# Kernel optimization log

Measured on AMD Instinct MI355X. Metric: run time of the kernel, lower is better.

The kernel has to match this reference:

```python
import jax, jax.numpy as jnp
from jax import lax
import numpy as np

B, IMG, PS = 64, 384, 16
DM, DS, DI = 96, 16, 96
DT_RANK = 6
NREP = 4
NCLS = 5
HP = IMG // PS            # 24 patches per side
N = HP * HP               # 576 tokens


def _ln(x, g, b):
    m = x.mean(-1, keepdims=True)
    v = ((x - m) ** 2).mean(-1, keepdims=True)
    return (x - m) * lax.rsqrt(v + 1e-5) * g + b


def setup_inputs() -> dict:
    key = jax.random.key(0)
    ks = jax.random.split(key, 16)
    nrm = lambda k, s: jax.random.normal(k, s, jnp.float32) * 0.02
    return {
        "x": jax.random.uniform(ks[0], (B, 3, IMG, IMG), jnp.float32),
        "W_pe": nrm(ks[1], (DM, 3, PS, PS)), "b_pe": jnp.zeros((DM,), jnp.float32),
        "W_vis": nrm(ks[2], (DM, 1)), "b_vis": jnp.zeros((1,), jnp.float32),
        "dn_g": jnp.ones((DM,), jnp.float32), "dn_b": jnp.zeros((DM,), jnp.float32),
        "W_gate": nrm(ks[3], (DM, DM)), "b_gate": jnp.zeros((DM,), jnp.float32),
        "ln_g": jnp.ones((DM,), jnp.float32), "ln_b": jnp.zeros((DM,), jnp.float32),
        "W_in": nrm(ks[4], (DM, 2 * DI)),
        "conv_w": nrm(ks[5], (DI, 1, 3)),
        "W_xproj": nrm(ks[6], (DI, DT_RANK + 2 * DS)),
        "W_dt": nrm(ks[7], (DT_RANK, DI)), "b_dt": jnp.full((DI,), -2.0, jnp.float32),
        "A_log": jnp.log(jnp.tile(jnp.arange(1, DS + 1, dtype=jnp.float32), (DI, 1))),
        "D": jnp.ones((DI,), jnp.float32),
        "W_out": nrm(ks[8], (DI, DM)),
        "hd_dw": nrm(ks[9], (DM, 1, 3, 3)),
        "bn_g": jnp.ones((DM,), jnp.float32), "bn_b": jnp.zeros((DM,), jnp.float32),
        "bn_m": jnp.zeros((DM,), jnp.float32), "bn_v": jnp.ones((DM,), jnp.float32),
        "W_heat": nrm(ks[10], (NCLS, DM)), "b_heat": jnp.full((NCLS,), -2.19, jnp.float32),
        "W_off": nrm(ks[11], (2, DM)), "b_off": jnp.zeros((2,), jnp.float32),
        "W_size": nrm(ks[12], (2, DM)), "b_size": jnp.zeros((2,), jnp.float32),
    }


def _forward(x, W_pe, b_pe, W_vis, b_vis, dn_g, dn_b, W_gate, b_gate,
             ln_g, ln_b, W_in, conv_w, W_xproj, W_dt, b_dt, A_log, D, W_out,
             hd_dw, bn_g, bn_b, bn_m, bn_v, W_heat, b_heat, W_off, b_off, W_size, b_size):
    # --- retinex preprocessing (single-scale, log domain) ---
    kblur = jnp.ones((3, 1, 5, 5), jnp.float32) / 25.0
    L = lax.conv_general_dilated(x, kblur, (1, 1), 'SAME',
                                 feature_group_count=3,
                                 dimension_numbers=('NCHW', 'OIHW', 'NCHW'))
    x = jnp.log1p(jnp.clip(x, 0.0)) - jnp.log1p(jnp.clip(L, 0.0))
    # --- patch embedding: strided conv -> tokens (B,N,DM) ---
    t = lax.conv_general_dilated(x, W_pe, (PS, PS), 'VALID',
                                 dimension_numbers=('NCHW', 'OIHW', 'NCHW'))
    t = t + b_pe[None, :, None, None]
    tokens = t.reshape(B, DM, N).transpose(0, 2, 1)
    # --- visibility estimator: per-token gate (B,N,1) ---
    vis = jax.nn.sigmoid(tokens @ W_vis + b_vis)
    # --- dual norm: LN + sigmoid gate ---
    tokens = _ln(tokens, dn_g, dn_b)
    norm_gate = jax.nn.sigmoid(tokens @ W_gate + b_gate)  # (B,N,DM)
    # --- weight-shared NC-SSM blocks ---
    A = -jnp.exp(A_log)  # (DI,DS)
    for _ in range(NREP):
        resid = tokens
        h = _ln(tokens, ln_g, ln_b)
        xz = h @ W_in                      # (B,N,2*DI)
        xin, z = xz[..., :DI], xz[..., DI:]
        # causal depthwise conv1d over sequence, kernel 3
        xc = xin.transpose(0, 2, 1)        # (B,DI,N)
        xc = lax.conv_general_dilated(xc, conv_w, (1,), [(2, 0)],
                                      feature_group_count=DI,
                                      dimension_numbers=('NCH', 'OIH', 'NCH'))
        xs = jax.nn.silu(xc.transpose(0, 2, 1))  # (B,N,DI)
        # selective-scan parameters
        proj = xs @ W_xproj                # (B,N,DT_RANK+2*DS)
        dt_raw = proj[..., :DT_RANK]
        Bc = proj[..., DT_RANK:DT_RANK + DS]
        Cc = proj[..., DT_RANK + DS:]
        dt = jax.nn.softplus(dt_raw @ W_dt + b_dt)  # (B,N,DI)
        # time-major scan
        def step(hst, inp):
            dt_t, B_t, C_t, x_t = inp      # (B,DI),(B,DS),(B,DS),(B,DI)
            dA = jnp.exp(dt_t[:, :, None] * A)                 # (B,DI,DS)
            hst = dA * hst + (dt_t * x_t)[:, :, None] * B_t[:, None, :]
            y = jnp.einsum('bds,bs->bd', hst, C_t)
            return hst, y
        h0 = jnp.zeros((B, DI, DS), jnp.float32)
        _, ys = lax.scan(step, h0, (dt.transpose(1, 0, 2), Bc.transpose(1, 0, 2),
                                    Cc.transpose(1, 0, 2), xs.transpose(1, 0, 2)))
        y = ys.transpose(1, 0, 2) + D * xs           # (B,N,DI)
        y = y * jax.nn.silu(z) * vis                  # gated by z and visibility
        tokens = resid + (y @ W_out) * norm_gate
    # --- CenterNet-style head ---
    f = tokens.transpose(0, 2, 1).reshape(B, DM, HP, HP)
    g = lax.conv_general_dilated(f, hd_dw, (1, 1), 'SAME',
                                 feature_group_count=DM,
                                 dimension_numbers=('NCHW', 'OIHW', 'NCHW'))
    g = (g - bn_m[None, :, None, None]) * lax.rsqrt(bn_v + 1e-5)[None, :, None, None]
    g = jax.nn.silu(g * bn_g[None, :, None, None] + bn_b[None, :, None, None])
    heat = jnp.einsum('bchw,oc->bohw', g, W_heat) + b_heat[None, :, None, None]
    off = jnp.einsum('bchw,oc->bohw', f, W_off) + b_off[None, :, None, None]
    size = jnp.einsum('bchw,oc->bohw', f, W_size) + b_size[None, :, None, None]
    return heat, off, size


def reference(x, W_pe, b_pe, W_vis, b_vis, dn_g, dn_b, W_gate, b_gate,
              ln_g, ln_b, W_in, conv_w, W_xproj, W_dt, b_dt, A_log, D, W_out,
              hd_dw, bn_g, bn_b, bn_m, bn_v, W_heat, b_heat, W_off, b_off, W_size, b_size):
    return _forward(x, W_pe, b_pe, W_vis, b_vis, dn_g, dn_b, W_gate, b_gate,
                    ln_g, ln_b, W_in, conv_w, W_xproj, W_dt, b_dt, A_log, D, W_out,
                    hd_dw, bn_g, bn_b, bn_m, bn_v, W_heat, b_heat, W_off, b_off,
                    W_size, b_size)
```

## Files before the change

kernel.cpp:

```cpp
#include <hip/hip_runtime.h>

#define DEVINL __device__ __forceinline__

typedef __attribute__((ext_vector_type(8))) short bf8v;
typedef __attribute__((ext_vector_type(4))) float f4v;

DEVINL float b2f(unsigned short u){ union{unsigned int i; float f;} x; x.i = ((unsigned int)u)<<16; return x.f; }
DEVINL unsigned short f2b(float f){ union{float f; unsigned int i;} x; x.f = f; unsigned int r = x.i + 0x7FFFu + ((x.i>>16)&1u); return (unsigned short)(r>>16); }
DEVINL float sigf(float v){ return 1.f/(1.f + __expf(-v)); }
DEVINL void unpack8(const uint4 u, float* d){
  d[0]=b2f((unsigned short)(u.x)); d[1]=b2f((unsigned short)(u.x>>16));
  d[2]=b2f((unsigned short)(u.y)); d[3]=b2f((unsigned short)(u.y>>16));
  d[4]=b2f((unsigned short)(u.z)); d[5]=b2f((unsigned short)(u.z>>16));
  d[6]=b2f((unsigned short)(u.w)); d[7]=b2f((unsigned short)(u.w>>16));
}
DEVINL uint4 pack8(const float* s){
  uint4 u;
  u.x = (unsigned int)f2b(s[0]) | ((unsigned int)f2b(s[1])<<16);
  u.y = (unsigned int)f2b(s[2]) | ((unsigned int)f2b(s[3])<<16);
  u.z = (unsigned int)f2b(s[4]) | ((unsigned int)f2b(s[5])<<16);
  u.w = (unsigned int)f2b(s[6]) | ((unsigned int)f2b(s[7])<<16);
  return u;
}
union FragU { uint4 u; bf8v v; };


#define WS_XLOG   ((size_t)0)
#define WS_TOK    ((size_t)56623104)
#define WS_VIS    ((size_t)70778880)
#define WS_WGT    ((size_t)70926336)
#define WS_WIT    ((size_t)70944768)
#define WS_WXT    ((size_t)70981632)
#define WS_WOT    ((size_t)71006208)
#define WS_AMAT   ((size_t)71024640)
#define WS_WPE    ((size_t)71030784)
#define WS_CW     ((size_t)71178240)
#define WS_BC     ((size_t)0)
#define WS_GATE   ((size_t)14155776)
#define WS_XSB    ((size_t)21233664)
#define WS_Y2     ((size_t)28311552)
#define WS_XIN    ((size_t)35389440)
#define WS_ZSV    ((size_t)42467328)
#define WS_DT     ((size_t)49545216)

#define PREP_STRIDE (128*256)
__global__ __launch_bounds__(256) void k_prep(
    const float* __restrict__ Wgate, const float* __restrict__ Win,
    const float* __restrict__ Wxproj, const float* __restrict__ Wdt,
    const float* __restrict__ Wout, const float* __restrict__ Alog,
    const float* __restrict__ Wpe, const float* __restrict__ convw,
    unsigned short* __restrict__ WgT, unsigned short* __restrict__ WiT,
    unsigned short* __restrict__ WxT, unsigned short* __restrict__ WoT,
    float* __restrict__ Amat, unsigned short* __restrict__ WpeB,
    float* __restrict__ cwsplit)
{
  int gtid = blockIdx.x*256 + threadIdx.x;
  for (int i = gtid; i < 9216; i += PREP_STRIDE){
    int n = i/96, k = i - n*96;
    WgT[n*96+k] = f2b(Wgate[k*96+n]);
    WoT[n*96+k] = f2b(Wout[k*96+n]);
  }
  for (int i = gtid; i < 18432; i += PREP_STRIDE){
    int n = i/96, k = i - n*96;
    WiT[n*96+k] = f2b(Win[k*192+n]);
  }
  for (int i = gtid; i < 12288; i += PREP_STRIDE){
    int n = i/96, k = i - n*96;
    if (n < 96){
      float s = 0.f;
      for (int r = 0; r < 6; ++r) s += Wxproj[k*38+r] * Wdt[r*96+n];
      WxT[n*96+k] = f2b(s);
    } else {
      WxT[n*96+k] = f2b(Wxproj[k*38 + 6 + (n-96)]);
    }
  }
  for (int i = gtid; i < 1536; i += PREP_STRIDE) Amat[i] = -__expf(Alog[i]);
  for (int i = gtid; i < 73728; i += PREP_STRIDE) WpeB[i] = f2b(Wpe[i]);
  for (int i = gtid; i < 96; i += PREP_STRIDE){
    cwsplit[i]       = convw[i*3+0];
    cwsplit[96+i]    = convw[i*3+1];
    cwsplit[192+i]   = convw[i*3+2];
  }
}

__global__ __launch_bounds__(256) void k_blur(const float* __restrict__ x,
                                              unsigned short* __restrict__ xlog)
{
  __shared__ unsigned short xt[12*384];
  __shared__ float vt[8*392];
  int bid = blockIdx.x;
  int tile = bid % 48; int bc = bid / 48; int c = bc % 3; int b = bc / 3;
  const float* xin = x + (size_t)(b*3 + c) * 147456;
  unsigned short* xout = xlog + (size_t)(b*3 + c) * 147456;
  int y0 = tile * 8;
  int tid = threadIdx.x;

  #pragma unroll
  for (int k = 0; k < 5; ++k){
    int idx = tid + k*256;
    if (idx < 1152){
      int r = idx / 96; int c4 = idx - r*96;
      int gy = y0 - 2 + r;
      float4 v = make_float4(0.f,0.f,0.f,0.f);
      if (gy >= 0 && gy < 384) v = *(const float4*)(xin + gy*384 + c4*4);
      ushort4 o; o.x=f2b(v.x); o.y=f2b(v.y); o.z=f2b(v.z); o.w=f2b(v.w);
      *(ushort4*)(xt + r*384 + c4*4) = o;
    }
  }
  if (tid < 64){
    int r = tid >> 3; int j = tid & 7;
    vt[r*392 + ((j < 4) ? j : (384 + j))] = 0.f;
  }
  __syncthreads();

  #pragma unroll
  for (int k = 0; k < 2; ++k){
    int unit = tid + k*256;
    if (unit < 384){
      int r = unit / 48; int c8 = unit - r*48;
      const unsigned short* base = xt + r*384 + c8*8;
      float acc[8]; float t[8];
      uint4 u0 = *(const uint4*)(base);
      unpack8(u0, acc);
      #pragma unroll
      for (int i = 1; i < 5; ++i){
        uint4 u = *(const uint4*)(base + i*384);
        unpack8(u, t);
        #pragma unroll
        for (int j = 0; j < 8; ++j) acc[j] += t[j];
      }
      float* vrow = vt + r*392 + 4 + c8*8;
      *(float4*)(vrow)   = make_float4(acc[0],acc[1],acc[2],acc[3]);
      *(float4*)(vrow+4) = make_float4(acc[4],acc[5],acc[6],acc[7]);
    }
  }
  __syncthreads();

  #pragma unroll
  for (int k = 0; k < 3; ++k){
    int unit = tid + k*256;
    int r = unit / 96; int c4 = unit - r*96;
    int base = r*392 + 4 + c4*4;
    float f[12];
    *(float4*)(f)   = *(const float4*)(vt + base - 4);
    *(float4*)(f+4) = *(const float4*)(vt + base);
    *(float4*)(f+8) = *(const float4*)(vt + base + 4);
    ushort4 xr = *(const ushort4*)(xt + (r+2)*384 + c4*4);
    const unsigned short* xrp = &xr.x;
    ushort4 o;
    unsigned short* op = &o.x;
    #pragma unroll
    for (int j = 0; j < 4; ++j){
      float s = f[2+j] + f[3+j] + f[4+j] + f[5+j] + f[6+j];
      float L = fmaxf(s * 0.04f, 0.f);
      float xv = fmaxf(b2f(xrp[j]), 0.f);
      op[j] = f2b(__logf(1.f + xv) - __logf(1.f + L));
    }
    *(ushort4*)(xout + (y0+r)*384 + c4*4) = o;
  }
}

__global__ __launch_bounds__(256) void k_patchln(
    const unsigned short* __restrict__ xlog, const unsigned short* __restrict__ WpeB,
    const float* __restrict__ bpe, const float* __restrict__ dng,
    const float* __restrict__ dnb, const float* __restrict__ Wvis,
    const float* __restrict__ bvis, float* __restrict__ tok, float* __restrict__ vis)
{
  int wid = threadIdx.x >> 6, lane = threadIdx.x & 63;
  int m0 = (blockIdx.x*4 + wid)*16;
  int l15 = lane & 15, q = lane >> 4;
  int ma0 = m0 + l15;
  int b0 = ma0/576; int r0 = ma0 - b0*576; int hp0 = r0/24; int wp0 = r0 - hp0*24;
  size_t base0 = (size_t)b0*442368 + (size_t)hp0*6144 + (size_t)wp0*16;
  f4v acc[6];
  #pragma unroll
  for (int j=0;j<6;++j)
    #pragma unroll
    for (int r=0;r<4;++r) acc[j][r] = 0.f;
  for (int ks = 0; ks < 24; ++ks){
    int k0 = ks*32 + q*8;
    int c  = k0 >> 8;
    int ph = (k0 >> 4) & 15;
    int pw = k0 & 15;
    size_t off = (size_t)c*147456 + (size_t)ph*384 + pw;
    bf8v a0 = *(const bf8v*)(xlog + base0 + off);
    #pragma unroll
    for (int nf = 0; nf < 6; ++nf){
      bf8v bb = *(const bf8v*)(WpeB + (size_t)(nf*16 + l15)*768 + k0);
      acc[nf] = __builtin_amdgcn_mfma_f32_16x16x32_bf16(a0, bb, acc[nf], 0, 0, 0);
    }
  }
  float v[6][4];
  float s[4], w[4], vd[4];
  #pragma unroll
  for (int r=0;r<4;++r){ s[r]=0.f; w[r]=0.f; vd[r]=0.f; }
  #pragma unroll
  for (int nf=0; nf<6; ++nf){
    int n = nf*16 + l15;
    float bp = bpe[n];
    float wv = Wvis[n];
    #pragma unroll
    for (int r=0;r<4;++r){
      float t = acc[nf][r] + bp;
      v[nf][r] = t;
      s[r] += t; w[r] += t*t; vd[r] += t*wv;
    }
  }
  #pragma unroll
  for (int off=1; off<16; off<<=1){
    #pragma unroll
    for (int r=0;r<4;++r){
      s[r]  += __shfl_xor(s[r],  off);
      w[r]  += __shfl_xor(w[r],  off);
      vd[r] += __shfl_xor(vd[r], off);
    }
  }
  float mu[4], rs[4];
  #pragma unroll
  for (int r=0;r<4;++r){
    mu[r] = s[r]*(1.f/96.f);
    rs[r] = rsqrtf(fmaxf(w[r]*(1.f/96.f)-mu[r]*mu[r], 0.f) + 1e-5f);
  }
  if (l15 == 0){
    #pragma unroll
    for (int r=0;r<4;++r) vis[m0 + q*4 + r] = sigf(vd[r] + bvis[0]);
  }
  #pragma unroll
  for (int nf=0; nf<6; ++nf){
    int n = nf*16 + l15;
    float g = dng[n], bb = dnb[n];
    #pragma unroll
    for (int r=0;r<4;++r)
      tok[(size_t)(m0 + q*4 + r)*96 + n] = (v[nf][r]-mu[r])*rs[r]*g + bb;
  }
}

__global__ __launch_bounds__(256) void k_lnfull(const float* __restrict__ tokp,
    const unsigned short* __restrict__ WgT, const float* __restrict__ bg,
    const float* __restrict__ lng, const float* __restrict__ lnb,
    const unsigned short* __restrict__ WiT, const float* __restrict__ vis,
    unsigned short* __restrict__ gate, unsigned short* __restrict__ xin,
    unsigned short* __restrict__ zsv)
{
  int wid = threadIdx.x >> 6, lane = threadIdx.x & 63;
  int gid = blockIdx.x*4 + wid;
  int tile = gid >> 1, half = gid & 1;
  int m0 = tile*16;
  int l15 = lane & 15, q = lane >> 4;
  int ma0 = m0 + l15;
  float a0v[24];
  float s1=0.f, w1=0.f;
  bf8v fa[3];
  #pragma unroll
  for (int ks = 0; ks < 3; ++ks){
    int k0 = ks*32 + q*8;
    float v0[8];
    #pragma unroll
    for (int h = 0; h < 2; ++h){
      float4 va = *(const float4*)(tokp + (size_t)ma0*96 + k0 + h*4);
      int o = ks*8 + h*4;
      a0v[o+0]=va.x; a0v[o+1]=va.y; a0v[o+2]=va.z; a0v[o+3]=va.w;
      v0[h*4+0]=va.x; v0[h*4+1]=va.y; v0[h*4+2]=va.z; v0[h*4+3]=va.w;
      s1 += (va.x+va.y)+(va.z+va.w);
      w1 += (va.x*va.x+va.y*va.y)+(va.z*va.z+va.w*va.w);
    }
    FragU U0; U0.u = pack8(v0);
    fa[ks] = U0.v;
  }
  s1 += __shfl_xor(s1, 16); s1 += __shfl_xor(s1, 32);
  w1 += __shfl_xor(w1, 16); w1 += __shfl_xor(w1, 32);
  float mu1 = s1*(1.f/96.f);
  float rs1 = rsqrtf(fmaxf(w1*(1.f/96.f)-mu1*mu1, 0.f) + 1e-5f);
  bf8v fb[3];
  #pragma unroll
  for (int ks = 0; ks < 3; ++ks){
    int k0 = ks*32 + q*8;
    float gv[8], bv[8];
    *(float4*)(gv)   = *(const float4*)(lng + k0);
    *(float4*)(gv+4) = *(const float4*)(lng + k0 + 4);
    *(float4*)(bv)   = *(const float4*)(lnb + k0);
    *(float4*)(bv+4) = *(const float4*)(lnb + k0 + 4);
    float v0[8];
    #pragma unroll
    for (int j = 0; j < 8; ++j)
      v0[j] = (a0v[ks*8+j]-mu1)*rs1*gv[j] + bv[j];
    FragU U0; U0.u = pack8(v0);
    fb[ks] = U0.v;
  }

  {
    f4v ag[3];
    #pragma unroll
    for (int j=0;j<3;++j)
      #pragma unroll
      for (int r=0;r<4;++r) ag[j][r] = 0.f;
    const bf8v* bpg = (const bf8v*)(WgT) + (size_t)l15*12 + q;
    #pragma unroll
    for (int ks = 0; ks < 3; ++ks)
      #pragma unroll
      for (int nf = 0; nf < 3; ++nf){
        bf8v bb = bpg[(half*3+nf)*192 + ks*4];
        ag[nf] = __builtin_amdgcn_mfma_f32_16x16x32_bf16(fa[ks], bb, ag[nf], 0, 0, 0);
      }
    #pragma unroll
    for (int nf=0; nf<3; ++nf)
      #pragma unroll
      for (int r=0; r<4; ++r){
        int m = m0 + q*4 + r;
        int n = (half*3+nf)*16 + l15;
        gate[(size_t)m*96 + n] = f2b(sigf(ag[nf][r] + bg[n]));
      }
  }

  {
    f4v aw[6];
    #pragma unroll
    for (int j=0;j<6;++j)
      #pragma unroll
      for (int r=0;r<4;++r) aw[j][r] = 0.f;
    const bf8v* bpw = (const bf8v*)(WiT) + (size_t)l15*12 + q;
    #pragma unroll
    for (int ks = 0; ks < 3; ++ks)
      #pragma unroll
      for (int nf = 0; nf < 6; ++nf){
        bf8v bb = bpw[(half*6+nf)*192 + ks*4];
        aw[nf] = __builtin_amdgcn_mfma_f32_16x16x32_bf16(fb[ks], bb, aw[nf], 0, 0, 0);
      }
    if (half == 0){
      #pragma unroll
      for (int nf=0; nf<6; ++nf)
        #pragma unroll
        for (int r=0; r<4; ++r){
          int m = m0 + q*4 + r;
          int n = nf*16 + l15;
          xin[(size_t)m*96 + n] = f2b(aw[nf][r]);
        }
    } else {
      #pragma unroll
      for (int nf=0; nf<6; ++nf)
        #pragma unroll
        for (int r=0; r<4; ++r){
          int m = m0 + q*4 + r;
          int n = nf*16 + l15;
          float v = aw[nf][r];
          float sgl = v * sigf(v);
          zsv[(size_t)m*96 + n] = f2b(sgl * vis[m]);
        }
    }
  }
}

template<bool DOLN>
__global__ __launch_bounds__(256) void k_woutln(
    const unsigned short* __restrict__ y2, const unsigned short* __restrict__ WoT,
    const unsigned short* __restrict__ gate,
    const float* __restrict__ lng, const float* __restrict__ lnb,
    const unsigned short* __restrict__ WiT, const float* __restrict__ vis,
    float* __restrict__ tok, unsigned short* __restrict__ xin,
    unsigned short* __restrict__ zsv)
{
  __shared__ float Sl[2][16][100];
  int wid = threadIdx.x >> 6, lane = threadIdx.x & 63;
  int gid = blockIdx.x*4 + wid;
  int tile = gid >> 1, half = gid & 1;
  int tl = wid >> 1;
  int m0 = tile*16;
  int l15 = lane & 15, q = lane >> 4;

  f4v acc[3];
  #pragma unroll
  for (int j=0;j<3;++j)
    #pragma unroll
    for (int r=0;r<4;++r) acc[j][r] = 0.f;
  const bf8v* a0p = (const bf8v*)(y2) + (size_t)(m0 + l15)*12 + q;
  const bf8v* bp  = (const bf8v*)(WoT) + (size_t)l15*12 + q;
  #pragma unroll
  for (int ks = 0; ks < 3; ++ks){
    bf8v a0 = a0p[ks*4];
    #pragma unroll
    for (int nf = 0; nf < 3; ++nf){
      bf8v bb = bp[(half*3+nf)*192 + ks*4];
      acc[nf] = __builtin_amdgcn_mfma_f32_16x16x32_bf16(a0, bb, acc[nf], 0, 0, 0);
    }
  }
  #pragma unroll
  for (int nf=0; nf<3; ++nf)
    #pragma unroll
    for (int r=0; r<4; ++r){
      int m = m0 + q*4 + r;
      int n = (half*3+nf)*16 + l15;
      size_t i = (size_t)m*96 + n;
      float tn = tok[i] + acc[nf][r] * b2f(gate[i]);
      tok[i] = tn;
      if constexpr (DOLN) Sl[tl][q*4+r][n] = tn;
    }

  if constexpr (DOLN){
    __syncthreads();
    int ma0 = m0 + l15;
    float a0v[24];
    float s0=0.f, w0=0.f;
    #pragma unroll
    for (int ks = 0; ks < 3; ++ks){
      int k0 = ks*32 + q*8;
      #pragma unroll
      for (int h = 0; h < 2; ++h){
        float4 va = *(const float4*)(&Sl[tl][l15][k0 + h*4]);
        int o = ks*8 + h*4;
        a0v[o+0]=va.x; a0v[o+1]=va.y; a0v[o+2]=va.z; a0v[o+3]=va.w;
        s0 += (va.x+va.y)+(va.z+va.w);
        w0 += (va.x*va.x+va.y*va.y)+(va.z*va.z+va.w*va.w);
      }
    }
    s0 += __shfl_xor(s0, 16); s0 += __shfl_xor(s0, 32);
    w0 += __shfl_xor(w0, 16); w0 += __shfl_xor(w0, 32);
    float mu0 = s0*(1.f/96.f);
    float rs0 = rsqrtf(fmaxf(w0*(1.f/96.f)-mu0*mu0, 0.f) + 1e-5f);
    bf8v fb[3];
    #pragma unroll
    for (int ks = 0; ks < 3; ++ks){
      int k0 = ks*32 + q*8;
      float gv[8], bv[8];
      *(float4*)(gv)   = *(const float4*)(lng + k0);
      *(float4*)(gv+4) = *(const float4*)(lng + k0 + 4);
      *(float4*)(bv)   = *(const float4*)(lnb + k0);
      *(float4*)(bv+4) = *(const float4*)(lnb + k0 + 4);
      float v0[8];
      #pragma unroll
      for (int j = 0; j < 8; ++j)
        v0[j] = (a0v[ks*8+j]-mu0)*rs0*gv[j] + bv[j];
      FragU U0; U0.u = pack8(v0);
      fb[ks] = U0.v;
    }
    f4v aw[6];
    #pragma unroll
    for (int j=0;j<6;++j)
      #pragma unroll
      for (int r=0;r<4;++r) aw[j][r] = 0.f;
    const bf8v* bpw = (const bf8v*)(WiT) + (size_t)l15*12 + q;
    #pragma unroll
    for (int ks = 0; ks < 3; ++ks)
      #pragma unroll
      for (int nf = 0; nf < 6; ++nf){
        bf8v bb = bpw[(half*6+nf)*192 + ks*4];
        aw[nf] = __builtin_amdgcn_mfma_f32_16x16x32_bf16(fb[ks], bb, aw[nf], 0, 0, 0);
      }
    if (half == 0){
      #pragma unroll
      for (int nf=0; nf<6; ++nf)
        #pragma unroll
        for (int r=0; r<4; ++r){
          int m = m0 + q*4 + r;
          int n = nf*16 + l15;
          xin[(size_t)m*96 + n] = f2b(aw[nf][r]);
        }
    } else {
      #pragma unroll
      for (int nf=0; nf<6; ++nf)
        #pragma unroll
        for (int r=0; r<4; ++r){
          int m = m0 + q*4 + r;
          int n = nf*16 + l15;
          float v = aw[nf][r];
          float sgl = v * sigf(v);
          zsv[(size_t)m*96 + n] = f2b(sgl * vis[m]);
        }
    }
  }
}

__global__ __launch_bounds__(256) void k_convxp(const unsigned short* __restrict__ xinb,
    const float* __restrict__ cwsplit, const unsigned short* __restrict__ BT,
    const float* __restrict__ bdt, unsigned short* __restrict__ xsb,
    unsigned short* __restrict__ dt, unsigned short* __restrict__ bc)
{
  int wid = threadIdx.x >> 6, lane = threadIdx.x & 63;
  int gid = blockIdx.x*4 + wid;
  int tile = gid >> 1, half = gid & 1;
  int m0 = tile*16;
  int nf0 = half*4;
  int l15 = lane & 15, q = lane >> 4;
  int ma0 = m0 + l15;
  int t0 = ma0 % 576;
  const float* cw0 = cwsplit;
  const float* cw1 = cwsplit + 96;
  const float* cw2 = cwsplit + 192;

  bf8v fa0[3];
  uint4 z4 = make_uint4(0,0,0,0);
  #pragma unroll
  for (int ks = 0; ks < 3; ++ks){
    int k0 = ks*32 + q*8;
    const unsigned short* r0p = xinb + (size_t)ma0*96 + k0;
    uint4 c0u  = *(const uint4*)(r0p);
    uint4 p10u = (t0 >= 1) ? *(const uint4*)(r0p - 96)  : z4;
    uint4 p20u = (t0 >= 2) ? *(const uint4*)(r0p - 192) : z4;
    float fc0[8], fp10[8], fp20[8];
    unpack8(c0u, fc0); unpack8(p10u, fp10); unpack8(p20u, fp20);
    float w0v[8], w1v[8], w2v[8];
    *(float4*)(w0v)   = *(const float4*)(cw0 + k0);
    *(float4*)(w0v+4) = *(const float4*)(cw0 + k0 + 4);
    *(float4*)(w1v)   = *(const float4*)(cw1 + k0);
    *(float4*)(w1v+4) = *(const float4*)(cw1 + k0 + 4);
    *(float4*)(w2v)   = *(const float4*)(cw2 + k0);
    *(float4*)(w2v+4) = *(const float4*)(cw2 + k0 + 4);
    float xs0[8];
    #pragma unroll
    for (int j = 0; j < 8; ++j){
      float v0 = w2v[j]*fc0[j] + w1v[j]*fp10[j] + w0v[j]*fp20[j];
      xs0[j] = v0 * sigf(v0);
    }
    FragU U0; U0.u = pack8(xs0);
    fa0[ks] = U0.v;
    if (half == 0) *(uint4*)(xsb + (size_t)ma0*96 + k0) = U0.u;
  }

  f4v acc[4];
  #pragma unroll
  for (int j=0;j<4;++j)
    #pragma unroll
    for (int r=0;r<4;++r) acc[j][r] = 0.f;
  const bf8v* bp = (const bf8v*)(BT) + (size_t)l15*12 + q;
  #pragma unroll
  for (int ks = 0; ks < 3; ++ks){
    #pragma unroll
    for (int nf = 0; nf < 4; ++nf){
      bf8v bb = bp[(nf0+nf)*192 + ks*4];
      acc[nf] = __builtin_amdgcn_mfma_f32_16x16x32_bf16(fa0[ks], bb, acc[nf], 0, 0, 0);
    }
  }
  #pragma unroll
  for (int nf=0; nf<4; ++nf)
    #pragma unroll
    for (int r=0; r<4; ++r){
      int m = m0 + q*4 + r;
      int n = (nf0+nf)*16 + l15;
      float v = acc[nf][r];
      if (n < 96){
        float xx = v + bdt[n];
        float sp = (xx > 20.f) ? xx : __logf(1.f + __expf(xx));
        dt[(size_t)m*96 + n] = f2b(sp);
      } else {
        bc[(size_t)m*32 + (n-96)] = f2b(v);
      }
    }
}

__global__ __launch_bounds__(512) void k_scan(const unsigned short* __restrict__ dt,
    const unsigned short* __restrict__ xsb, const unsigned short* __restrict__ bc,
    const unsigned short* __restrict__ zsv, const float* __restrict__ Amat,
    const float* __restrict__ Dw, unsigned short* __restrict__ y2)
{
  __shared__ float Ul[32*16*17];
  __shared__ float Sl[32*16];
  int b = blockIdx.x / 6; int dg = blockIdx.x - b*6;
  int tid = threadIdx.x;
  int c = tid >> 4; int dl = tid & 15; int d = dg*16 + dl;
  float As[16];
  #pragma unroll
  for (int s = 0; s < 16; s += 4){
    float4 t4 = *(const float4*)(Amat + d*16 + s);
    As[s]=t4.x; As[s+1]=t4.y; As[s+2]=t4.z; As[s+3]=t4.w;
  }
  bool fast = true;
  #pragma unroll
  for (int s = 0; s < 16; ++s)
    fast = fast && (fabsf(As[s] + (float)(s+1)) <= 2e-5f*(float)(s+1));

  float h[16];
  #pragma unroll
  for (int s=0;s<16;++s) h[s]=0.f;
  float sdt = 0.f;
  int tbase = b*576 + c*18;
  if (fast){
    for (int i = 0; i < 18; ++i){
      size_t m = (size_t)(tbase + i);
      float dtv = b2f(dt[m*96 + d]);
      float dtx = dtv * b2f(xsb[m*96 + d]);
      const uint4* bp = (const uint4*)(bc + m*32);
      float Bv[16];
      unpack8(bp[0], Bv); unpack8(bp[1], Bv+8);
      sdt += dtv;
      float w1=__expf(-dtv), w2=w1*w1, w3=w2*w1, w4=w2*w2;
      float w5=w4*w1, w6=w4*w2, w7=w4*w3, w8=w4*w4;
      float w9=w8*w1, w10=w8*w2, w11=w8*w3, w12=w8*w4;
      float w13=w8*w5, w14=w8*w6, w15=w8*w7, w16=w8*w8;
      float dA[16]={w1,w2,w3,w4,w5,w6,w7,w8,w9,w10,w11,w12,w13,w14,w15,w16};
      #pragma unroll
      for (int s=0;s<16;++s) h[s] = dA[s]*h[s] + dtx*Bv[s];
    }
  } else {
    for (int i = 0; i < 18; ++i){
      size_t m = (size_t)(tbase + i);
      float dtv = b2f(dt[m*96 + d]);
      float dtx = dtv * b2f(xsb[m*96 + d]);
      const uint4* bp = (const uint4*)(bc + m*32);
      float Bv[16];
      unpack8(bp[0], Bv); unpack8(bp[1], Bv+8);
      sdt += dtv;
      #pragma unroll
      for (int s=0;s<16;++s) h[s] = __expf(As[s]*dtv)*h[s] + dtx*Bv[s];
    }
  }
  {
    int base = (c*16 + dl)*17;
    #pragma unroll
    for (int s=0;s<16;++s) Ul[base + s] = h[s];
    Sl[c*16 + dl] = sdt;
  }
  __syncthreads();
  if (tid < 256){
    int dl2 = tid >> 4, s2 = tid & 15;
    float A2 = Amat[(dg*16 + dl2)*16 + s2];
    float hh = 0.f;
    for (int cc = 0; cc < 32; ++cc){
      float u = Ul[(cc*16 + dl2)*17 + s2];
      float ss = Sl[cc*16 + dl2];
      hh = __expf(A2*ss)*hh + u;
      Ul[(cc*16 + dl2)*17 + s2] = hh;
    }
  }
  __syncthreads();
  if (c == 0){
    #pragma unroll
    for (int s=0;s<16;++s) h[s] = 0.f;
  } else {
    int base = ((c-1)*16 + dl)*17;
    #pragma unroll
    for (int s=0;s<16;++s) h[s] = Ul[base + s];
  }
  float Dd = Dw[d];
  if (fast){
    for (int i = 0; i < 18; ++i){
      size_t m = (size_t)(tbase + i);
      float dtv = b2f(dt[m*96 + d]);
      float xv = b2f(xsb[m*96 + d]);
      float dtx = dtv * xv;
      const uint4* bp = (const uint4*)(bc + m*32);
      float Bv[16], Cv[16];
      unpack8(bp[0], Bv); unpack8(bp[1], Bv+8);
      unpack8(bp[2], Cv); unpack8(bp[3], Cv+8);
      float w1=__expf(-dtv), w2=w1*w1, w3=w2*w1, w4=w2*w2;
      float w5=w4*w1, w6=w4*w2, w7=w4*w3, w8=w4*w4;
      float w9=w8*w1, w10=w8*w2, w11=w8*w3, w12=w8*w4;
      float w13=w8*w5, w14=w8*w6, w15=w8*w7, w16=w8*w8;
      float dA[16]={w1,w2,w3,w4,w5,w6,w7,w8,w9,w10,w11,w12,w13,w14,w15,w16};
      float p0=0.f,p1=0.f,p2=0.f,p3=0.f;
      #pragma unroll
      for (int s=0;s<16;s+=4){
        h[s+0] = dA[s+0]*h[s+0] + dtx*Bv[s+0]; p0 += h[s+0]*Cv[s+0];
        h[s+1] = dA[s+1]*h[s+1] + dtx*Bv[s+1]; p1 += h[s+1]*Cv[s+1];
        h[s+2] = dA[s+2]*h[s+2] + dtx*Bv[s+2]; p2 += h[s+2]*Cv[s+2];
        h[s+3] = dA[s+3]*h[s+3] + dtx*Bv[s+3]; p3 += h[s+3]*Cv[s+3];
      }
      float y = (p0+p1) + (p2+p3);
      float yv = (y + Dd*xv) * b2f(zsv[m*96 + d]);
      y2[m*96 + d] = f2b(yv);
    }
  } else {
    for (int i = 0; i < 18; ++i){
      size_t m = (size_t)(tbase + i);
      float dtv = b2f(dt[m*96 + d]);
      float xv = b2f(xsb[m*96 + d]);
      float dtx = dtv * xv;
      const uint4* bp = (const uint4*)(bc + m*32);
      float Bv[16], Cv[16];
      unpack8(bp[0], Bv); unpack8(bp[1], Bv+8);
      unpack8(bp[2], Cv); unpack8(bp[3], Cv+8);
      float p0=0.f,p1=0.f,p2=0.f,p3=0.f;
      #pragma unroll
      for (int s=0;s<16;s+=4){
        h[s+0] = __expf(As[s+0]*dtv)*h[s+0] + dtx*Bv[s+0]; p0 += h[s+0]*Cv[s+0];
        h[s+1] = __expf(As[s+1]*dtv)*h[s+1] + dtx*Bv[s+1]; p1 += h[s+1]*Cv[s+1];
        h[s+2] = __expf(As[s+2]*dtv)*h[s+2] + dtx*Bv[s+2]; p2 += h[s+2]*Cv[s+2];
        h[s+3] = __expf(As[s+3]*dtv)*h[s+3] + dtx*Bv[s+3]; p3 += h[s+3]*Cv[s+3];
      }
      float y = (p0+p1) + (p2+p3);
      float yv = (y + Dd*xv) * b2f(zsv[m*96 + d]);
      y2[m*96 + d] = f2b(yv);
    }
  }
}

__global__ __launch_bounds__(256) void k_head(const float* __restrict__ tokens,
    const float* __restrict__ hdw, const float* __restrict__ bng,
    const float* __restrict__ bnb, const float* __restrict__ bnm,
    const float* __restrict__ bnv, const float* __restrict__ Wheat,
    const float* __restrict__ bheat, const float* __restrict__ Woff,
    const float* __restrict__ boff, const float* __restrict__ Wsize,
    const float* __restrict__ bsize, float* __restrict__ out)
{
  __shared__ float ft[3*2304];
  __shared__ float act[2304];
  int b = blockIdx.x / 24; int h = blockIdx.x - b*24;
  for (int i = threadIdx.x; i < 3*2304; i += 256){
    int rr = i / 2304; int j = i - rr*2304;
    int hh = h + rr - 1;
    float v = 0.f;
    if (hh >= 0 && hh < 24) v = tokens[((size_t)b*576 + hh*24)*96 + j];
    ft[rr*2304 + j] = v;
  }
  __syncthreads();
  for (int i = threadIdx.x; i < 2304; i += 256){
    int w = i / 96; int cc = i - w*96;
    float g = 0.f;
    #pragma unroll
    for (int dh = 0; dh < 3; ++dh){
      #pragma unroll
      for (int dw = 0; dw < 3; ++dw){
        int ww = w + dw - 1;
        if (ww >= 0 && ww < 24) g += ft[dh*2304 + ww*96 + cc] * hdw[cc*9 + dh*3 + dw];
      }
    }
    float gn = (g - bnm[cc]) * rsqrtf(bnv[cc] + 1e-5f);
    float a = gn * bng[cc] + bnb[cc];
    act[i] = a * sigf(a);
  }
  __syncthreads();
  int tid = threadIdx.x;
  if (tid < 120){
    int o = tid / 24; int w = tid - o*24;
    float s = 0.f;
    for (int cc = 0; cc < 96; ++cc) s += act[w*96 + cc] * Wheat[o*96 + cc];
    s += bheat[o];
    out[(size_t)b*2880 + o*576 + h*24 + w] = s;
  } else if (tid >= 128 && tid < 224){
    int idx = tid - 128; int o2 = idx / 24; int w = idx - o2*24;
    const float* W = (o2 < 2) ? Woff : Wsize;
    int o = o2 & 1;
    float s = 0.f;
    for (int cc = 0; cc < 96; ++cc) s += ft[2304 + w*96 + cc] * W[o*96 + cc];
    s += ((o2 < 2) ? boff : bsize)[o];
    size_t baseo = (o2 < 2) ? (size_t)184320 : (size_t)258048;
    out[baseo + (size_t)b*1152 + o*576 + h*24 + w] = s;
  }
}

extern "C" void kernel_launch(void* const* d_in, const int* in_sizes, int n_in,
                              void* d_out, int out_size, void* d_ws, size_t ws_size,
                              hipStream_t stream)
{
  (void)in_sizes; (void)n_in; (void)out_size; (void)ws_size;
  const float* x      = (const float*)d_in[0];
  const float* Wpe    = (const float*)d_in[1];
  const float* bpe    = (const float*)d_in[2];
  const float* Wvis   = (const float*)d_in[3];
  const float* bvis   = (const float*)d_in[4];
  const float* dng    = (const float*)d_in[5];
  const float* dnb    = (const float*)d_in[6];
  const float* Wgate  = (const float*)d_in[7];
  const float* bgate  = (const float*)d_in[8];
  const float* lng    = (const float*)d_in[9];
  const float* lnb    = (const float*)d_in[10];
  const float* Win    = (const float*)d_in[11];
  const float* convw  = (const float*)d_in[12];
  const float* Wxproj = (const float*)d_in[13];
  const float* Wdt    = (const float*)d_in[14];
  const float* bdt    = (const float*)d_in[15];
  const float* Alog   = (const float*)d_in[16];
  const float* Dw     = (const float*)d_in[17];
  const float* Wout   = (const float*)d_in[18];
  const float* hddw   = (const float*)d_in[19];
  const float* bng    = (const float*)d_in[20];
  const float* bnb    = (const float*)d_in[21];
  const float* bnm    = (const float*)d_in[22];
  const float* bnv    = (const float*)d_in[23];
  const float* Wheat  = (const float*)d_in[24];
  const float* bheat  = (const float*)d_in[25];
  const float* Woff   = (const float*)d_in[26];
  const float* boff   = (const float*)d_in[27];
  const float* Wsize  = (const float*)d_in[28];
  const float* bsize  = (const float*)d_in[29];
  float* out = (float*)d_out;

  char* ws = (char*)d_ws;
  unsigned short* xlog  = (unsigned short*)(ws + WS_XLOG);
  float*          tok   = (float*)(ws + WS_TOK);
  float*          vis   = (float*)(ws + WS_VIS);
  unsigned short* WgT   = (unsigned short*)(ws + WS_WGT);
  unsigned short* WiT   = (unsigned short*)(ws + WS_WIT);
  unsigned short* WxT   = (unsigned short*)(ws + WS_WXT);
  unsigned short* WoT   = (unsigned short*)(ws + WS_WOT);
  float*          Amat  = (float*)(ws + WS_AMAT);
  unsigned short* WpeB  = (unsigned short*)(ws + WS_WPE);
  float*          cwsp  = (float*)(ws + WS_CW);
  unsigned short* bcb   = (unsigned short*)(ws + WS_BC);
  unsigned short* gate  = (unsigned short*)(ws + WS_GATE);
  unsigned short* xsb   = (unsigned short*)(ws + WS_XSB);
  unsigned short* y2    = (unsigned short*)(ws + WS_Y2);
  unsigned short* xinb  = (unsigned short*)(ws + WS_XIN);
  unsigned short* zsvb  = (unsigned short*)(ws + WS_ZSV);
  unsigned short* dtb   = (unsigned short*)(ws + WS_DT);

  k_prep<<<128, 256, 0, stream>>>(Wgate, Win, Wxproj, Wdt, Wout, Alog, Wpe, convw,
                                  WgT, WiT, WxT, WoT, Amat, WpeB, cwsp);
  k_blur<<<9216, 256, 0, stream>>>(x, xlog);
  k_patchln<<<576, 256, 0, stream>>>(xlog, WpeB, bpe, dng, dnb, Wvis, bvis, tok, vis);
  k_lnfull<<<1152, 256, 0, stream>>>(tok, WgT, bgate, lng, lnb, WiT, vis,
                                     gate, xinb, zsvb);

  for (int rep = 0; rep < 4; ++rep){
    k_convxp<<<1152, 256, 0, stream>>>(xinb, cwsp, WxT, bdt, xsb, dtb, bcb);
    k_scan<<<384, 512, 0, stream>>>(dtb, xsb, bcb, zsvb, Amat, Dw, y2);
    if (rep < 3)
      k_woutln<true><<<1152, 256, 0, stream>>>(y2, WoT, gate, lng, lnb, WiT, vis,
                                               tok, xinb, zsvb);
    else
      k_woutln<false><<<1152, 256, 0, stream>>>(y2, WoT, gate, lng, lnb, WiT, vis,
                                                tok, xinb, zsvb);
  }

  k_head<<<1536, 256, 0, stream>>>(tok, hddw, bng, bnb, bnm, bnv,
                                   Wheat, bheat, Woff, boff, Wsize, bsize, out);
}
```

Before: 671.7 us.

## Fuse patch embed with gate and in-projection; keep blur tile in fp32

Adds k_patchfull, which runs the patch-embedding MFMA, the first LayerNorm, the visibility score, the gate GEMM and the in-projection GEMM in one kernel. Each block splits the output columns across two wave halves and shares the per-token rows through LDS. This removes one launch and the tok round trip to global memory, but it only runs when the workspace is large enough, because the intermediate buffers move to new offsets so they do not overlap xlog. The blur kernel now stages the input tile in fp32 instead of bf16 and computes the vertical 5-tap sum as a running sum, which drops the pack and unpack work in exchange for doubling the shared-memory footprint.

```diff
diff --git a/kernel.cpp b/kernel.cpp
--- a/kernel.cpp
+++ b/kernel.cpp
@@ -24,24 +24,6 @@
 }
 union FragU { uint4 u; bf8v v; };
 
-
-#define WS_XLOG   ((size_t)0)
-#define WS_TOK    ((size_t)56623104)
-#define WS_VIS    ((size_t)70778880)
-#define WS_WGT    ((size_t)70926336)
-#define WS_WIT    ((size_t)70944768)
-#define WS_WXT    ((size_t)70981632)
-#define WS_WOT    ((size_t)71006208)
-#define WS_AMAT   ((size_t)71024640)
-#define WS_WPE    ((size_t)71030784)
-#define WS_CW     ((size_t)71178240)
-#define WS_BC     ((size_t)0)
-#define WS_GATE   ((size_t)14155776)
-#define WS_XSB    ((size_t)21233664)
-#define WS_Y2     ((size_t)28311552)
-#define WS_XIN    ((size_t)35389440)
-#define WS_ZSV    ((size_t)42467328)
-#define WS_DT     ((size_t)49545216)
 
 #define PREP_STRIDE (128*256)
 __global__ __launch_bounds__(256) void k_prep(
@@ -86,7 +68,7 @@
 __global__ __launch_bounds__(256) void k_blur(const float* __restrict__ x,
                                               unsigned short* __restrict__ xlog)
 {
-  __shared__ unsigned short xt[12*384];
+  __shared__ float xt[12*384];
   __shared__ float vt[8*392];
   int bid = blockIdx.x;
   int tile = bid % 48; int bc = bid / 48; int c = bc % 3; int b = bc / 3;
@@ -103,8 +85,7 @@
       int gy = y0 - 2 + r;
       float4 v = make_float4(0.f,0.f,0.f,0.f);
       if (gy >= 0 && gy < 384) v = *(const float4*)(xin + gy*384 + c4*4);
-      ushort4 o; o.x=f2b(v.x); o.y=f2b(v.y); o.z=f2b(v.z); o.w=f2b(v.w);
-      *(ushort4*)(xt + r*384 + c4*4) = o;
+      *(float4*)(xt + r*384 + c4*4) = v;
     }
   }
   if (tid < 64){
@@ -115,23 +96,17 @@
 
   #pragma unroll
   for (int k = 0; k < 2; ++k){
-    int unit = tid + k*256;
-    if (unit < 384){
-      int r = unit / 48; int c8 = unit - r*48;
-      const unsigned short* base = xt + r*384 + c8*8;
-      float acc[8]; float t[8];
-      uint4 u0 = *(const uint4*)(base);
-      unpack8(u0, acc);
-      #pragma unroll
-      for (int i = 1; i < 5; ++i){
-        uint4 u = *(const uint4*)(base + i*384);
-        unpack8(u, t);
-        #pragma unroll
-        for (int j = 0; j < 8; ++j) acc[j] += t[j];
-      }
-      float* vrow = vt + r*392 + 4 + c8*8;
-      *(float4*)(vrow)   = make_float4(acc[0],acc[1],acc[2],acc[3]);
-      *(float4*)(vrow+4) = make_float4(acc[4],acc[5],acc[6],acc[7]);
+    int cc = tid + k*256;
+    if (cc < 384){
+      float x0 = xt[cc], x1 = xt[384+cc], x2 = xt[768+cc],
+            x3 = xt[1152+cc], x4 = xt[1536+cc];
+      float vs = ((x0+x1)+(x2+x3))+x4;
+      vt[4+cc] = vs;
+      #pragma unroll
+      for (int r = 1; r < 8; ++r){
+        vs += xt[(r+4)*384+cc] - xt[(r-1)*384+cc];
+        vt[r*392+4+cc] = vs;
+      }
     }
   }
   __syncthreads();
@@ -145,16 +120,16 @@
     *(float4*)(f)   = *(const float4*)(vt + base - 4);
     *(float4*)(f+4) = *(const float4*)(vt + base);
     *(float4*)(f+8) = *(const float4*)(vt + base + 4);
-    ushort4 xr = *(const ushort4*)(xt + (r+2)*384 + c4*4);
-    const unsigned short* xrp = &xr.x;
+    float xv[4];
+    *(float4*)(xv) = *(const float4*)(xt + (r+2)*384 + c4*4);
     ushort4 o;
     unsigned short* op = &o.x;
     #pragma unroll
     for (int j = 0; j < 4; ++j){
       float s = f[2+j] + f[3+j] + f[4+j] + f[5+j] + f[6+j];
       float L = fmaxf(s * 0.04f, 0.f);
-      float xv = fmaxf(b2f(xrp[j]), 0.f);
-      op[j] = f2b(__logf(1.f + xv) - __logf(1.f + L));
+      float xc = fmaxf(xv[j], 0.f);
+      op[j] = f2b(__logf(1.f + xc) - __logf(1.f + L));
     }
     *(ushort4*)(xout + (y0+r)*384 + c4*4) = o;
   }
@@ -287,7 +262,6 @@
     FragU U0; U0.u = pack8(v0);
     fb[ks] = U0.v;
   }
-
   {
     f4v ag[3];
     #pragma unroll
@@ -311,7 +285,6 @@
         gate[(size_t)m*96 + n] = f2b(sigf(ag[nf][r] + bg[n]));
       }
   }
-
   {
     f4v aw[6];
     #pragma unroll
@@ -345,6 +318,196 @@
           float v = aw[nf][r];
           float sgl = v * sigf(v);
           zsv[(size_t)m*96 + n] = f2b(sgl * vis[m]);
+        }
+    }
+  }
+}
+
+__global__ __launch_bounds__(256) void k_patchfull(
+    const unsigned short* __restrict__ xlog, const unsigned short* __restrict__ WpeB,
+    const float* __restrict__ bpe,
+    const float* __restrict__ dng, const float* __restrict__ dnb,
+    const float* __restrict__ Wvis, const float* __restrict__ bvis,
+    const unsigned short* __restrict__ WgT, const float* __restrict__ bg,
+    const float* __restrict__ lng, const float* __restrict__ lnb,
+    const unsigned short* __restrict__ WiT,
+    float* __restrict__ tok, unsigned short* __restrict__ gate,
+    float* __restrict__ vis, unsigned short* __restrict__ xin,
+    unsigned short* __restrict__ zsv)
+{
+  __shared__ float Sl[2][16][100];
+  __shared__ float Vl[2][16];
+  int wid = threadIdx.x >> 6, lane = threadIdx.x & 63;
+  int gid = blockIdx.x*4 + wid;
+  int tile = gid >> 1, half = gid & 1;
+  int tl = wid >> 1;
+  int m0 = tile*16;
+  int l15 = lane & 15, q = lane >> 4;
+  int ma0 = m0 + l15;
+
+  {
+    int b0 = ma0/576; int r0 = ma0 - b0*576; int hp0 = r0/24; int wp0 = r0 - hp0*24;
+    size_t base0 = (size_t)b0*442368 + (size_t)hp0*6144 + (size_t)wp0*16;
+    f4v acc[3];
+    #pragma unroll
+    for (int j=0;j<3;++j)
+      #pragma unroll
+      for (int r=0;r<4;++r) acc[j][r] = 0.f;
+    for (int ks = 0; ks < 24; ++ks){
+      int k0 = ks*32 + q*8;
+      int c  = k0 >> 8;
+      int ph = (k0 >> 4) & 15;
+      int pw = k0 & 15;
+      size_t off = (size_t)c*147456 + (size_t)ph*384 + pw;
+      bf8v a0 = *(const bf8v*)(xlog + base0 + off);
+      #pragma unroll
+      for (int nf = 0; nf < 3; ++nf){
+        bf8v bb = *(const bf8v*)(WpeB + (size_t)((half*3+nf)*16 + l15)*768 + k0);
+        acc[nf] = __builtin_amdgcn_mfma_f32_16x16x32_bf16(a0, bb, acc[nf], 0, 0, 0);
+      }
+    }
+    #pragma unroll
+    for (int nf=0; nf<3; ++nf)
+      #pragma unroll
+      for (int r=0; r<4; ++r){
+        int n = (half*3+nf)*16 + l15;
+        Sl[tl][q*4+r][n] = acc[nf][r] + bpe[n];
+      }
+  }
+  __syncthreads();
+
+  float a0v[24];
+  float s0=0.f, w0=0.f, vd=0.f;
+  #pragma unroll
+  for (int ks = 0; ks < 3; ++ks){
+    int k0 = ks*32 + q*8;
+    #pragma unroll
+    for (int h = 0; h < 2; ++h){
+      float4 va = *(const float4*)(&Sl[tl][l15][k0 + h*4]);
+      float4 wv = *(const float4*)(Wvis + k0 + h*4);
+      int o = ks*8 + h*4;
+      a0v[o+0]=va.x; a0v[o+1]=va.y; a0v[o+2]=va.z; a0v[o+3]=va.w;
+      s0 += (va.x+va.y)+(va.z+va.w);
+      w0 += (va.x*va.x+va.y*va.y)+(va.z*va.z+va.w*va.w);
+      vd += (va.x*wv.x+va.y*wv.y)+(va.z*wv.z+va.w*wv.w);
+    }
+  }
+  s0 += __shfl_xor(s0, 16); s0 += __shfl_xor(s0, 32);
+  w0 += __shfl_xor(w0, 16); w0 += __shfl_xor(w0, 32);
+  vd += __shfl_xor(vd, 16); vd += __shfl_xor(vd, 32);
+  float mu0 = s0*(1.f/96.f);
+  float rs0 = rsqrtf(fmaxf(w0*(1.f/96.f)-mu0*mu0, 0.f) + 1e-5f);
+  if (half == 0 && q == 0){
+    float vv = sigf(vd + bvis[0]);
+    vis[ma0] = vv;
+    Vl[tl][l15] = vv;
+  }
+
+  bf8v fa[3];
+  float s1=0.f, w1=0.f;
+  #pragma unroll
+  for (int ks = 0; ks < 3; ++ks){
+    int k0 = ks*32 + q*8;
+    float gv[8], bv[8];
+    *(float4*)(gv)   = *(const float4*)(dng + k0);
+    *(float4*)(gv+4) = *(const float4*)(dng + k0 + 4);
+    *(float4*)(bv)   = *(const float4*)(dnb + k0);
+    *(float4*)(bv+4) = *(const float4*)(dnb + k0 + 4);
+    float v0[8];
+    #pragma unroll
+    for (int j = 0; j < 8; ++j){
+      float v = (a0v[ks*8+j]-mu0)*rs0*gv[j] + bv[j];
+      v0[j] = v;
+      a0v[ks*8+j] = v;
+      s1 += v; w1 += v*v;
+    }
+    if (half == 0){
+      *(float4*)(tok + (size_t)ma0*96 + k0)     = make_float4(v0[0],v0[1],v0[2],v0[3]);
+      *(float4*)(tok + (size_t)ma0*96 + k0 + 4) = make_float4(v0[4],v0[5],v0[6],v0[7]);
+    }
+    FragU U0; U0.u = pack8(v0);
+    fa[ks] = U0.v;
+  }
+
+  {
+    f4v ag[3];
+    #pragma unroll
+    for (int j=0;j<3;++j)
+      #pragma unroll
+      for (int r=0;r<4;++r) ag[j][r] = 0.f;
+    const bf8v* bpg = (const bf8v*)(WgT) + (size_t)l15*12 + q;
+    #pragma unroll
+    for (int ks = 0; ks < 3; ++ks)
+      #pragma unroll
+      for (int nf = 0; nf < 3; ++nf){
+        bf8v bb = bpg[(half*3+nf)*192 + ks*4];
+        ag[nf] = __builtin_amdgcn_mfma_f32_16x16x32_bf16(fa[ks], bb, ag[nf], 0, 0, 0);
+      }
+    #pragma unroll
+    for (int nf=0; nf<3; ++nf)
+      #pragma unroll
+      for (int r=0; r<4; ++r){
+        int m = m0 + q*4 + r;
+        int n = (half*3+nf)*16 + l15;
+        gate[(size_t)m*96 + n] = f2b(sigf(ag[nf][r] + bg[n]));
+      }
+  }
+
+  s1 += __shfl_xor(s1, 16); s1 += __shfl_xor(s1, 32);
+  w1 += __shfl_xor(w1, 16); w1 += __shfl_xor(w1, 32);
+  float mu1 = s1*(1.f/96.f);
+  float rs1 = rsqrtf(fmaxf(w1*(1.f/96.f)-mu1*mu1, 0.f) + 1e-5f);
+  bf8v fb[3];
+  #pragma unroll
+  for (int ks = 0; ks < 3; ++ks){
+    int k0 = ks*32 + q*8;
+    float gv[8], bv[8];
+    *(float4*)(gv)   = *(const float4*)(lng + k0);
+    *(float4*)(gv+4) = *(const float4*)(lng + k0 + 4);
+    *(float4*)(bv)   = *(const float4*)(lnb + k0);
+    *(float4*)(bv+4) = *(const float4*)(lnb + k0 + 4);
+    float v0[8];
+    #pragma unroll
+    for (int j = 0; j < 8; ++j)
+      v0[j] = (a0v[ks*8+j]-mu1)*rs1*gv[j] + bv[j];
+    FragU U0; U0.u = pack8(v0);
+    fb[ks] = U0.v;
+  }
+  __syncthreads();
+
+  {
+    f4v aw[6];
+    #pragma unroll
+    for (int j=0;j<6;++j)
+      #pragma unroll
+      for (int r=0;r<4;++r) aw[j][r] = 0.f;
+    const bf8v* bpw = (const bf8v*)(WiT) + (size_t)l15*12 + q;
+    #pragma unroll
+    for (int ks = 0; ks < 3; ++ks)
+      #pragma unroll
+      for (int nf = 0; nf < 6; ++nf){
+        bf8v bb = bpw[(half*6+nf)*192 + ks*4];
+        aw[nf] = __builtin_amdgcn_mfma_f32_16x16x32_bf16(fb[ks], bb, aw[nf], 0, 0, 0);
+      }
+    if (half == 0){
+      #pragma unroll
+      for (int nf=0; nf<6; ++nf)
+        #pragma unroll
+        for (int r=0; r<4; ++r){
+          int m = m0 + q*4 + r;
+          int n = nf*16 + l15;
+          xin[(size_t)m*96 + n] = f2b(aw[nf][r]);
+        }
+    } else {
+      #pragma unroll
+      for (int nf=0; nf<6; ++nf)
+        #pragma unroll
+        for (int r=0; r<4; ++r){
+          int m = m0 + q*4 + r;
+          int n = nf*16 + l15;
+          float v = aw[nf][r];
+          float s = v * sigf(v);
+          zsv[(size_t)m*96 + n] = f2b(s * Vl[tl][q*4+r]);
         }
     }
   }
@@ -740,7 +903,7 @@
                               void* d_out, int out_size, void* d_ws, size_t ws_size,
                               hipStream_t stream)
 {
-  (void)in_sizes; (void)n_in; (void)out_size; (void)ws_size;
+  (void)in_sizes; (void)n_in; (void)out_size;
   const float* x      = (const float*)d_in[0];
   const float* Wpe    = (const float*)d_in[1];
   const float* bpe    = (const float*)d_in[2];
@@ -773,31 +936,58 @@
   const float* bsize  = (const float*)d_in[29];
   float* out = (float*)d_out;
 
+  const bool big = ws_size >= (size_t)120324096;
   char* ws = (char*)d_ws;
-  unsigned short* xlog  = (unsigned short*)(ws + WS_XLOG);
-  float*          tok   = (float*)(ws + WS_TOK);
-  float*          vis   = (float*)(ws + WS_VIS);
-  unsigned short* WgT   = (unsigned short*)(ws + WS_WGT);
-  unsigned short* WiT   = (unsigned short*)(ws + WS_WIT);
-  unsigned short* WxT   = (unsigned short*)(ws + WS_WXT);
-  unsigned short* WoT   = (unsigned short*)(ws + WS_WOT);
-  float*          Amat  = (float*)(ws + WS_AMAT);
-  unsigned short* WpeB  = (unsigned short*)(ws + WS_WPE);
-  float*          cwsp  = (float*)(ws + WS_CW);
-  unsigned short* bcb   = (unsigned short*)(ws + WS_BC);
-  unsigned short* gate  = (unsigned short*)(ws + WS_GATE);
-  unsigned short* xsb   = (unsigned short*)(ws + WS_XSB);
-  unsigned short* y2    = (unsigned short*)(ws + WS_Y2);
-  unsigned short* xinb  = (unsigned short*)(ws + WS_XIN);
-  unsigned short* zsvb  = (unsigned short*)(ws + WS_ZSV);
-  unsigned short* dtb   = (unsigned short*)(ws + WS_DT);
+
+  size_t o_xlog = 0;
+  size_t o_tok  = 56623104;
+  size_t o_vis  = 70778880;
+  size_t o_wgt  = 70926336;
+  size_t o_wit  = 70944768;
+  size_t o_wxt  = 70981632;
+  size_t o_wot  = 71006208;
+  size_t o_amat = 71024640;
+  size_t o_wpe  = 71030784;
+  size_t o_cw   = 71178240;
+  size_t o_gate, o_xin, o_zsv, o_xsb, o_y2, o_dt, o_bc;
+  if (big){
+    o_gate = 75497472;  o_xin = 82575360;  o_zsv = 89653248;
+    o_xsb  = 96731136;  o_y2  = 103809024; o_dt  = 110886912; o_bc = 117964800;
+  } else {
+    o_bc   = 0;         o_gate = 14155776; o_xsb = 21233664;
+    o_y2   = 28311552;  o_xin  = 35389440; o_zsv = 42467328;  o_dt = 49545216;
+  }
+
+  unsigned short* xlog  = (unsigned short*)(ws + o_xlog);
+  float*          tok   = (float*)(ws + o_tok);
+  float*          vis   = (float*)(ws + o_vis);
+  unsigned short* WgT   = (unsigned short*)(ws + o_wgt);
+  unsigned short* WiT   = (unsigned short*)(ws + o_wit);
+  unsigned short* WxT   = (unsigned short*)(ws + o_wxt);
+  unsigned short* WoT   = (unsigned short*)(ws + o_wot);
+  float*          Amat  = (float*)(ws + o_amat);
+  unsigned short* WpeB  = (unsigned short*)(ws + o_wpe);
+  float*          cwsp  = (float*)(ws + o_cw);
+  unsigned short* gate  = (unsigned short*)(ws + o_gate);
+  unsigned short* xinb  = (unsigned short*)(ws + o_xin);
+  unsigned short* zsvb  = (unsigned short*)(ws + o_zsv);
+  unsigned short* xsb   = (unsigned short*)(ws + o_xsb);
+  unsigned short* y2    = (unsigned short*)(ws + o_y2);
+  unsigned short* dtb   = (unsigned short*)(ws + o_dt);
+  unsigned short* bcb   = (unsigned short*)(ws + o_bc);
 
   k_prep<<<128, 256, 0, stream>>>(Wgate, Win, Wxproj, Wdt, Wout, Alog, Wpe, convw,
                                   WgT, WiT, WxT, WoT, Amat, WpeB, cwsp);
   k_blur<<<9216, 256, 0, stream>>>(x, xlog);
-  k_patchln<<<576, 256, 0, stream>>>(xlog, WpeB, bpe, dng, dnb, Wvis, bvis, tok, vis);
-  k_lnfull<<<1152, 256, 0, stream>>>(tok, WgT, bgate, lng, lnb, WiT, vis,
-                                     gate, xinb, zsvb);
+  if (big){
+    k_patchfull<<<1152, 256, 0, stream>>>(xlog, WpeB, bpe, dng, dnb, Wvis, bvis,
+                                          WgT, bgate, lng, lnb, WiT,
+                                          tok, gate, vis, xinb, zsvb);
+  } else {
+    k_patchln<<<576, 256, 0, stream>>>(xlog, WpeB, bpe, dng, dnb, Wvis, bvis, tok, vis);
+    k_lnfull<<<1152, 256, 0, stream>>>(tok, WgT, bgate, lng, lnb, WiT, vis,
+                                       gate, xinb, zsvb);
+  }
 
   for (int rep = 0; rep < 4; ++rep){
     k_convxp<<<1152, 256, 0, stream>>>(xinb, cwsp, WxT, bdt, xsb, dtb, bcb);
```

Result: no change. 660.7 us (-1.6%).
